# Optimization experiments

Hardware: AMD Instinct MI355X
Metric: run time of the kernel (lower is better)

## Reference

```python
import jax, jax.numpy as jnp
import numpy as np

B, S, D = 8, 2048, 128

def setup_inputs() -> dict:
    key = jax.random.key(0)
    kq, kk, kv, km = jax.random.split(key, 4)
    q = jax.random.normal(kq, (B, S, D), dtype=jnp.float32)
    k = jax.random.normal(kk, (B, S, D), dtype=jnp.float32)
    v = jax.random.normal(kv, (B, S, D), dtype=jnp.float32)
    mask = jax.random.randint(km, (B, S), 0, 2).astype(bool)  # True = masked out
    return {"q": q, "k": k, "v": v, "mask": mask}

def reference(q, k, v, mask):
    scaler = np.sqrt(D).astype(np.float32)
    # score[b, i, j] = <q_i, k_j> / sqrt(d_k)
    score = jnp.einsum('bik,bjk->bij', q, k) / scaler
    score = score - jnp.max(score, axis=-1, keepdims=True)
    e = jnp.exp(score)
    # mask is (B, S_kv): broadcast across query positions, zero out masked keys
    e = jnp.where(mask[:, None, :], 0.0, e)
    a = e / jnp.sum(e, axis=-1, keepdims=True)
    c = jnp.einsum('bij,bjd->bid', a, v)
    return c
```

## Files before the change

kernel.cpp:

```cpp
#include <hip/hip_runtime.h>
#include <hip/hip_fp16.h>
#include <math.h>

typedef __attribute__((ext_vector_type(8))) short short8;
typedef __attribute__((ext_vector_type(16))) float floatx16;
typedef __attribute__((ext_vector_type(2))) __bf16 bf16x2;
typedef __attribute__((ext_vector_type(2))) unsigned int uint2v;

namespace {
constexpr int Bn = 8;
constexpr int Sn = 2048;
constexpr int Dn = 128;
constexpr int BQ = 128;
constexpr int BK = 64;
constexpr int QTILES = Sn / BQ;
constexpr int NKB = Sn / BK;
constexpr int ROWS = Bn * Sn;
constexpr int NSPLIT = 4;
constexpr float SC2 = 0.12753102063642597f;
constexpr float DEFER_THR = 8.0f;
constexpr int TILE_USH = BK * Dn;
}

#if __has_builtin(__builtin_amdgcn_exp2f)
#define EXP2(x) __builtin_amdgcn_exp2f(x)
#else
#define EXP2(x) exp2f(x)
#endif

__device__ __forceinline__ unsigned short f2bf(float x) {
  union { float f; unsigned u; } a; a.f = x;
  unsigned r = a.u + 0x7fffu + ((a.u >> 16) & 1u);
  return (unsigned short)(r >> 16);
}

__device__ __forceinline__ unsigned pack2bf(float x, float y) {
  union { bf16x2 b; unsigned u; } c;
  c.b[0] = (__bf16)x; c.b[1] = (__bf16)y;
  return c.u;
}

__device__ __forceinline__ uint2v pl32swap(unsigned a, unsigned b, int h) {
#if __has_builtin(__builtin_amdgcn_permlane32_swap)
  (void)h;
  return __builtin_amdgcn_permlane32_swap(a, b, false, false);
#else
  unsigned ax = __shfl_xor((int)a, 32);
  unsigned bx = __shfl_xor((int)b, 32);
  uint2v r;
  r[0] = h ? bx : a;
  r[1] = h ? b : ax;
  return r;
#endif
}

__device__ __forceinline__ void gl_lds16(const void* g, void* l, int lane) {
#if __has_builtin(__builtin_amdgcn_global_load_lds)
  (void)lane;
  __builtin_amdgcn_global_load_lds((const __attribute__((address_space(1))) unsigned int*)g,
                                   (__attribute__((address_space(3))) unsigned int*)l, 16, 0, 0);
#else
  *(float4*)((char*)l + lane * 16) = *(const float4*)g;
#endif
}

__global__ __launch_bounds__(256)
void mask_scan(const unsigned char* __restrict__ mraw,
               unsigned short* __restrict__ idxg, int* __restrict__ cntg,
               float* __restrict__ mb2g) {
  __shared__ int sc[256];
  const int b = blockIdx.x;
  const int t = threadIdx.x;

  unsigned wv = ((const unsigned int*)mraw)[t];
  int any1  = __syncthreads_or((wv & 0x0000ff00u) ? 1 : 0);
  int any23 = __syncthreads_or((wv & 0xffff0000u) ? 1 : 0);
  const int mlayout = any1 ? 1 : (any23 ? 2 : 0);

  const int s0 = t * 8;
  const int gbase = b * Sn + s0;
  bool ms[8];
  if (mlayout == 1) {
    #pragma unroll
    for (int i = 0; i < 8; ++i) ms[i] = mraw[gbase + i] != 0;
  } else if (mlayout == 2) {
    const float* mf = (const float*)mraw;
    #pragma unroll
    for (int i = 0; i < 8; ++i) ms[i] = mf[gbase + i] != 0.0f;
  } else {
    const int* mi = (const int*)mraw;
    #pragma unroll
    for (int i = 0; i < 8; ++i) ms[i] = mi[gbase + i] != 0;
  }

  int c = 0;
  #pragma unroll
  for (int i = 0; i < 8; ++i) c += ms[i] ? 0 : 1;
  sc[t] = c;
  __syncthreads();
  for (int off = 1; off < 256; off <<= 1) {
    int v = (t >= off) ? sc[t - off] : 0;
    __syncthreads();
    sc[t] += v;
    __syncthreads();
  }
  const int incl = sc[t];
  const int total = sc[255];
  int pos = incl - c;
  #pragma unroll
  for (int i = 0; i < 8; ++i)
    if (!ms[i]) idxg[b * Sn + (pos++)] = (unsigned short)(s0 + i);
  if (t == 0) cntg[b] = total;
  #pragma unroll
  for (int i = 0; i < 8; ++i)
    mb2g[b * Sn + s0 + i] = (s0 + i < total) ? 0.0f : -1e30f;
}

__global__ __launch_bounds__(256)
void prep(const float* __restrict__ kg, const float* __restrict__ vg,
          const unsigned short* __restrict__ idxg, const int* __restrict__ cntg,
          unsigned short* __restrict__ Kpg, unsigned short* __restrict__ Vpg) {
  __shared__ __align__(16) float Vf[16 * 136];
  const int p = blockIdx.x;
  const int b = p >> 7, qq = p & 127;
  const int kb = qq >> 2, k16 = qq & 3;
  const int t = threadIdx.x;

  const int cnt = cntg[b];
  const int padded = (cnt + 63) & ~63;
  const int slot0 = kb * 64 + k16 * 16;
  if (slot0 >= padded) return;

  const int j  = t >> 4;
  const int o8 = t & 15;
  const int sl = slot0 + j;
  const bool real = sl < cnt;

  float4 a, bq, va, vb;
  if (real) {
    const int srow = idxg[b * Sn + sl];
    const size_t base = ((size_t)(b * Sn + srow)) * 32 + o8 * 2;
    a  = ((const float4*)kg)[base]; bq = ((const float4*)kg)[base + 1];
    va = ((const float4*)vg)[base]; vb = ((const float4*)vg)[base + 1];
  } else {
    a = bq = va = vb = make_float4(0.f, 0.f, 0.f, 0.f);
  }

  {
    union { unsigned u[4]; short8 s8; } pk;
    pk.u[0] = pack2bf(a.x, a.y);   pk.u[1] = pack2bf(a.z, a.w);
    pk.u[2] = pack2bf(bq.x, bq.y); pk.u[3] = pack2bf(bq.z, bq.w);
    const int jl = k16 * 16 + j;
    *(short8*)(Kpg + (size_t)(b * NKB + kb) * TILE_USH + jl * 128 + ((o8 ^ (jl & 7)) * 8)) = pk.s8;
  }
  {
    *(float4*)&Vf[j * 136 + o8 * 8]     = va;
    *(float4*)&Vf[j * 136 + o8 * 8 + 4] = vb;
  }
  __syncthreads();
  {
    const int d = t >> 1, h = t & 1;
    union { unsigned u[4]; short8 s8; } pv;
    #pragma unroll
    for (int i = 0; i < 4; ++i)
      pv.u[i] = pack2bf(Vf[(h * 8 + 2 * i) * 136 + d], Vf[(h * 8 + 2 * i + 1) * 136 + d]);
    const int og = k16 * 2 + h;
    *(short8*)(Vpg + (size_t)(b * NKB + kb) * TILE_USH + d * 64 + ((og ^ (d & 7)) * 8)) = pv.s8;
  }
}


__device__ __forceinline__ void stage_tile(const char* gsrc, char* ldst,
                                           int stagebase, int L) {
  #pragma unroll
  for (int i = 0; i < 4; ++i) {
    const int off = stagebase + i * 1024;
    gl_lds16(gsrc + off + L * 16, ldst + off, L);
  }
}

__device__ __forceinline__ void qk_tile(const unsigned short* __restrict__ Kc,
                                        int q, int h, int sw,
                                        const short8 (&qh)[8], const short8 (&ql)[8],
                                        floatx16 (&s)[2]) {
  #pragma unroll
  for (int kg = 0; kg < 2; ++kg)
    #pragma unroll
    for (int r = 0; r < 16; ++r) s[kg][r] = 0.0f;
  #pragma unroll
  for (int kstep = 0; kstep < 8; ++kstep) {
    const int ko = ((kstep * 2 + h) ^ sw) * 8;
    #pragma unroll
    for (int kg = 0; kg < 2; ++kg) {
      short8 kf = *(const short8*)&Kc[(kg * 32 + q) * 128 + ko];
      s[kg] = __builtin_amdgcn_mfma_f32_32x32x16_bf16(kf, qh[kstep], s[kg], 0, 0, 0);
      s[kg] = __builtin_amdgcn_mfma_f32_32x32x16_bf16(kf, ql[kstep], s[kg], 0, 0, 0);
    }
  }
}

__device__ __forceinline__ void tile_body(
    int kbc, int kbN,
    const unsigned short* __restrict__ Kread, unsigned short* Kdst,
    const unsigned short* __restrict__ Vread, unsigned short* Vdst,
    const char* ktile, const char* vtile, int stagebase, int L,
    const float* __restrict__ mbrow,
    int q, int h, int sw,
    const short8 (&qh)[8], const short8 (&ql)[8],
    floatx16 (&sCur)[2], floatx16 (&sNxt)[2],
    floatx16 (&O32)[4], float& m_i, float& l_i, float& mtrue) {
  __syncthreads();

  if (kbc + 2 < kbN)
    stage_tile(ktile + (size_t)(kbc + 2) * (TILE_USH * 2), (char*)Kdst, stagebase, L);
  const bool hasNext = (kbc + 1 < kbN);
  if (hasNext)
    stage_tile(vtile + (size_t)(kbc + 1) * (TILE_USH * 2), (char*)Vdst, stagebase, L);

  if (hasNext)
    qk_tile(Kread, q, h, sw, qh, ql, sNxt);

  const float4* mb4 = (const float4*)(mbrow + kbc * BK);
  float4 mbv[2][4];
  #pragma unroll
  for (int kg = 0; kg < 2; ++kg)
    #pragma unroll
    for (int ro = 0; ro < 4; ++ro) mbv[kg][ro] = mb4[kg * 8 + ro * 2 + h];

  #pragma unroll
  for (int kg = 0; kg < 2; ++kg)
    #pragma unroll
    for (int ro = 0; ro < 4; ++ro) {
      float4 f = mbv[kg][ro];
      sCur[kg][4 * ro + 0] = fmaf(sCur[kg][4 * ro + 0], SC2, f.x);
      sCur[kg][4 * ro + 1] = fmaf(sCur[kg][4 * ro + 1], SC2, f.y);
      sCur[kg][4 * ro + 2] = fmaf(sCur[kg][4 * ro + 2], SC2, f.z);
      sCur[kg][4 * ro + 3] = fmaf(sCur[kg][4 * ro + 3], SC2, f.w);
    }
  float mxp[4] = {-INFINITY, -INFINITY, -INFINITY, -INFINITY};
  #pragma unroll
  for (int kg = 0; kg < 2; ++kg)
    #pragma unroll
    for (int r = 0; r < 16; ++r) mxp[r & 3] = fmaxf(mxp[r & 3], sCur[kg][r]);
  float mx = fmaxf(fmaxf(mxp[0], mxp[1]), fmaxf(mxp[2], mxp[3]));
  mx = fmaxf(mx, __shfl_xor(mx, 32));
  mtrue = fmaxf(mtrue, mx);

  float mnew;
  if (__all(mx <= m_i + DEFER_THR)) {
    mnew = m_i;
  } else {
    mnew = fmaxf(m_i, mx);
    const float alpha = EXP2(m_i - mnew);
    l_i *= alpha;
    #pragma unroll
    for (int dg = 0; dg < 4; ++dg)
      #pragma unroll
      for (int r = 0; r < 16; ++r) O32[dg][r] *= alpha;
  }

  float rsp[4] = {0.f, 0.f, 0.f, 0.f};
  #pragma unroll
  for (int kg = 0; kg < 2; ++kg)
    #pragma unroll
    for (int r = 0; r < 16; ++r) {
      float e = EXP2(sCur[kg][r] - mnew);
      sCur[kg][r] = e;
      rsp[r & 3] += e;
    }
  float rs = (rsp[0] + rsp[1]) + (rsp[2] + rsp[3]);
  rs += __shfl_xor(rs, 32);
  l_i += rs;
  m_i = mnew;

  unsigned xw[2][4][2];
  #pragma unroll
  for (int kg = 0; kg < 2; ++kg)
    #pragma unroll
    for (int m = 0; m < 4; ++m) {
      xw[kg][m][0] = pack2bf(sCur[kg][4 * m + 0], sCur[kg][4 * m + 1]);
      xw[kg][m][1] = pack2bf(sCur[kg][4 * m + 2], sCur[kg][4 * m + 3]);
    }
  unsigned pfw[4][4];
  #pragma unroll
  for (int kg = 0; kg < 2; ++kg)
    #pragma unroll
    for (int j = 0; j < 2; ++j)
      #pragma unroll
      for (int c2 = 0; c2 < 2; ++c2) {
        uint2v r = pl32swap(xw[kg][2 * j][c2], xw[kg][2 * j + 1][c2], h);
        pfw[kg * 2 + j][c2]     = r[0];
        pfw[kg * 2 + j][2 + c2] = r[1];
      }

  __builtin_amdgcn_s_setprio(1);
  #pragma unroll
  for (int k2 = 0; k2 < 4; ++k2) {
    const int ko = ((k2 * 2 + h) ^ sw) * 8;
    union { unsigned u[4]; short8 s8; } pw;
    pw.u[0] = pfw[k2][0]; pw.u[1] = pfw[k2][1];
    pw.u[2] = pfw[k2][2]; pw.u[3] = pfw[k2][3];
    #pragma unroll
    for (int dg = 0; dg < 4; ++dg) {
      short8 vf = *(const short8*)&Vread[(dg * 32 + q) * 64 + ko];
      O32[dg] = __builtin_amdgcn_mfma_f32_32x32x16_bf16(vf, pw.s8, O32[dg], 0, 0, 0);
    }
  }
  __builtin_amdgcn_s_setprio(0);
}

template<int SPLIT, bool DIRECT>
__global__ __launch_bounds__(256, 2)
void attn_fwd(const float* __restrict__ qg,
              const unsigned short* __restrict__ Kpg,
              const unsigned short* __restrict__ Vpg,
              const float* __restrict__ mb2g,
              const int* __restrict__ cntg,
              float* __restrict__ outg, __half* __restrict__ Op,
              float* __restrict__ Mp, float* __restrict__ Lp) {
  __shared__ __align__(16) unsigned short Khi[2][TILE_USH];
  __shared__ __align__(16) unsigned short Vt[2][TILE_USH];

  const int tid = threadIdx.x;
  const int bid = blockIdx.x;
  const int b   = bid & 7;
  const int q0  = ((bid >> 3) & (QTILES - 1)) * BQ;
  const int s   = bid >> 7;
  const int w   = tid >> 6;
  const int L   = tid & 63;
  const int q   = L & 31;
  const int h   = L >> 5;
  const int sw  = q & 7;

  const int cnt = cntg[b];
  const int nt  = (cnt + 63) >> 6;
  const int kb0 = (s * nt) / SPLIT;
  const int kbN = ((s + 1) * nt) / SPLIT;
  const int T   = kbN - kb0;

  const int row = b * Sn + q0 + w * 32 + q;

  if (T <= 0) {
    if constexpr (DIRECT) {
      float* orow = outg + (size_t)row * Dn;
      float4 z = make_float4(0.f, 0.f, 0.f, 0.f);
      #pragma unroll
      for (int dg = 0; dg < 4; ++dg)
        #pragma unroll
        for (int ro = 0; ro < 4; ++ro) *(float4*)&orow[dg * 32 + 8 * ro + 4 * h] = z;
    } else {
      __half* orow = Op + ((size_t)s * ROWS + row) * Dn;
      uint2 z; z.x = 0u; z.y = 0u;
      #pragma unroll
      for (int dg = 0; dg < 4; ++dg)
        #pragma unroll
        for (int ro = 0; ro < 4; ++ro) *(uint2*)&orow[dg * 32 + 8 * ro + 4 * h] = z;
      if (h == 0) { Mp[s * ROWS + row] = -INFINITY; Lp[s * ROWS + row] = 0.0f; }
    }
    return;
  }

  const char* ktile = (const char*)(Kpg + (size_t)b * NKB * TILE_USH);
  const char* vtile = (const char*)(Vpg + (size_t)b * NKB * TILE_USH);
  const float* mbrow = mb2g + b * Sn;
  const int stagebase = w * 4096;

  short8 qh[8], ql[8];
  {
    const float* qrow = qg + (size_t)row * Dn;
    #pragma unroll
    for (int kstep = 0; kstep < 8; ++kstep) {
      float4 f0 = *(const float4*)(qrow + kstep * 16 + h * 8);
      float4 f1 = *(const float4*)(qrow + kstep * 16 + h * 8 + 4);
      float xs[8] = {f0.x, f0.y, f0.z, f0.w, f1.x, f1.y, f1.z, f1.w};
      #pragma unroll
      for (int j = 0; j < 8; ++j) {
        unsigned short hi = f2bf(xs[j]);
        union { unsigned u; float f; } hv; hv.u = ((unsigned)hi) << 16;
        qh[kstep][j] = (short)hi;
        ql[kstep][j] = (short)f2bf(xs[j] - hv.f);
      }
    }
  }

  float m_i = -INFINITY, l_i = 0.0f;
  float mtrue = -INFINITY;
  floatx16 O32[4];
  #pragma unroll
  for (int dg = 0; dg < 4; ++dg)
    #pragma unroll
    for (int r = 0; r < 16; ++r) O32[dg][r] = 0.0f;

  stage_tile(ktile + (size_t)kb0 * (TILE_USH * 2), (char*)Khi[0], stagebase, L);
  stage_tile(vtile + (size_t)kb0 * (TILE_USH * 2), (char*)Vt[0], stagebase, L);
  __syncthreads();
  if (kb0 + 1 < kbN)
    stage_tile(ktile + (size_t)(kb0 + 1) * (TILE_USH * 2), (char*)Khi[1], stagebase, L);

  floatx16 sA[2], sB[2];
  qk_tile(Khi[0], q, h, sw, qh, ql, sA);

  int kb = kb0;
  for (; kb + 2 <= kbN; kb += 2) {
    tile_body(kb, kbN, Khi[1], Khi[0], Vt[0], Vt[1], ktile, vtile, stagebase, L,
              mbrow, q, h, sw, qh, ql, sA, sB, O32, m_i, l_i, mtrue);
    tile_body(kb + 1, kbN, Khi[0], Khi[1], Vt[1], Vt[0], ktile, vtile, stagebase, L,
              mbrow, q, h, sw, qh, ql, sB, sA, O32, m_i, l_i, mtrue);
  }
  if (kb < kbN)
    tile_body(kb, kbN, Khi[1], Khi[0], Vt[0], Vt[1], ktile, vtile, stagebase, L,
              mbrow, q, h, sw, qh, ql, sA, sB, O32, m_i, l_i, mtrue);

  if constexpr (DIRECT) {
    const float inv = 1.0f / l_i;
    float* orow = outg + (size_t)row * Dn;
    #pragma unroll
    for (int dg = 0; dg < 4; ++dg)
      #pragma unroll
      for (int ro = 0; ro < 4; ++ro) {
        float4 f = make_float4(O32[dg][4 * ro] * inv,     O32[dg][4 * ro + 1] * inv,
                               O32[dg][4 * ro + 2] * inv, O32[dg][4 * ro + 3] * inv);
        *(float4*)&orow[dg * 32 + 8 * ro + 4 * h] = f;
      }
  } else {
    const float fin = EXP2(m_i - mtrue);
    __half* orow = Op + ((size_t)s * ROWS + row) * Dn;
    #pragma unroll
    for (int dg = 0; dg < 4; ++dg)
      #pragma unroll
      for (int ro = 0; ro < 4; ++ro) {
        union { __half2 h2[2]; uint2 u; } pk;
        pk.h2[0] = __floats2half2_rn(O32[dg][4 * ro] * fin,     O32[dg][4 * ro + 1] * fin);
        pk.h2[1] = __floats2half2_rn(O32[dg][4 * ro + 2] * fin, O32[dg][4 * ro + 3] * fin);
        *(uint2*)&orow[dg * 32 + 8 * ro + 4 * h] = pk.u;
      }
    if (h == 0) {
      Mp[s * ROWS + row] = mtrue;
      Lp[s * ROWS + row] = l_i * fin;
    }
  }
}

__global__ __launch_bounds__(256)
void attn_combine(const __half* __restrict__ Op, const float* __restrict__ Mp,
                  const float* __restrict__ Lp, float4* __restrict__ out4) {
  const int gid = blockIdx.x * 256 + threadIdx.x;
  const int row = gid >> 5;
  const int c4  = gid & 31;
  float ms[NSPLIT];
  float m = -INFINITY;
  #pragma unroll
  for (int s = 0; s < NSPLIT; ++s) { ms[s] = Mp[s * ROWS + row]; m = fmaxf(m, ms[s]); }
  float l = 0.0f;
  float4 acc = make_float4(0.f, 0.f, 0.f, 0.f);
  #pragma unroll
  for (int s = 0; s < NSPLIT; ++s) {
    float wgt = EXP2(ms[s] - m);
    l = fmaf(Lp[s * ROWS + row], wgt, l);
    union { uint2 u; __half2 h2[2]; } pk;
    pk.u = ((const uint2*)Op)[(size_t)(s * ROWS + row) * 32 + c4];
    float2 f0 = __half22float2(pk.h2[0]);
    float2 f1 = __half22float2(pk.h2[1]);
    acc.x = fmaf(f0.x, wgt, acc.x);
    acc.y = fmaf(f0.y, wgt, acc.y);
    acc.z = fmaf(f1.x, wgt, acc.z);
    acc.w = fmaf(f1.y, wgt, acc.w);
  }
  float inv = 1.0f / l;
  out4[(size_t)row * 32 + c4] = make_float4(acc.x * inv, acc.y * inv, acc.z * inv, acc.w * inv);
}

extern "C" void kernel_launch(void* const* d_in, const int* in_sizes, int n_in,
                              void* d_out, int out_size, void* d_ws, size_t ws_size,
                              hipStream_t stream) {
  const float* q = (const float*)d_in[0];
  const float* k = (const float*)d_in[1];
  const float* v = (const float*)d_in[2];
  const unsigned char* m = (const unsigned char*)d_in[3];
  float* out = (float*)d_out;
  (void)in_sizes; (void)n_in; (void)out_size;

  constexpr size_t OPB = (size_t)NSPLIT * ROWS * Dn * sizeof(__half);
  constexpr size_t MLB = (size_t)NSPLIT * ROWS * sizeof(float);
  constexpr size_t KPB = (size_t)Bn * NKB * TILE_USH * 2;
  constexpr size_t MBB = (size_t)ROWS * sizeof(float);
  constexpr size_t CNTB = 64;
  constexpr size_t IDXB = (size_t)Bn * Sn * sizeof(unsigned short);

  char* ws = (char*)d_ws;
  if (ws_size >= OPB + 2 * MLB + 2 * KPB + MBB + CNTB + IDXB) {
    __half* Op = (__half*)ws;
    float* Mp = (float*)(ws + OPB);
    float* Lp = (float*)(ws + OPB + MLB);
    unsigned short* Kp = (unsigned short*)(ws + OPB + 2 * MLB);
    unsigned short* Vp = (unsigned short*)(ws + OPB + 2 * MLB + KPB);
    float* mb2 = (float*)(ws + OPB + 2 * MLB + 2 * KPB);
    int* cnt = (int*)(ws + OPB + 2 * MLB + 2 * KPB + MBB);
    unsigned short* idx = (unsigned short*)(ws + OPB + 2 * MLB + 2 * KPB + MBB + CNTB);
    mask_scan<<<dim3(Bn), dim3(256), 0, stream>>>(m, idx, cnt, mb2);
    prep<<<dim3(Bn * NKB * 4), dim3(256), 0, stream>>>(k, v, idx, cnt, Kp, Vp);
    attn_fwd<NSPLIT, false><<<dim3(Bn * QTILES * NSPLIT), dim3(256), 0, stream>>>(
        q, Kp, Vp, mb2, cnt, out, Op, Mp, Lp);
    attn_combine<<<dim3(ROWS * 32 / 256), dim3(256), 0, stream>>>(
        Op, Mp, Lp, (float4*)out);
  } else if (ws_size >= 2 * KPB + MBB + CNTB + IDXB) {
    unsigned short* Kp = (unsigned short*)ws;
    unsigned short* Vp = (unsigned short*)(ws + KPB);
    float* mb2 = (float*)(ws + 2 * KPB);
    int* cnt = (int*)(ws + 2 * KPB + MBB);
    unsigned short* idx = (unsigned short*)(ws + 2 * KPB + MBB + CNTB);
    mask_scan<<<dim3(Bn), dim3(256), 0, stream>>>(m, idx, cnt, mb2);
    prep<<<dim3(Bn * NKB * 4), dim3(256), 0, stream>>>(k, v, idx, cnt, Kp, Vp);
    attn_fwd<1, true><<<dim3(Bn * QTILES), dim3(256), 0, stream>>>(
        q, Kp, Vp, mb2, cnt, out, nullptr, nullptr, nullptr);
  }
}
```

Baseline: 110.1 us.

## Fuse mask scan into prep kernel and compute key padding mask inline

Removes the separate mask_scan launch: every prep block now redoes the per-batch prefix scan over the mask and keeps only the 16 compacted indices it needs in shared memory. The attention kernel drops the per-tile mask-bias loads and derives the padding bias from the valid-key count, using a plain scale on full tiles. This saves one kernel launch, a serial dependency and the global idx/mb2 traffic, at the cost of repeating the scan in 1024 blocks.

New measurement: 116.3 us. 5.7% more time.

```diff
diff --git a/kernel.cpp b/kernel.cpp
--- a/kernel.cpp
+++ b/kernel.cpp
@@ -65,11 +65,16 @@
 }
 
 __global__ __launch_bounds__(256)
-void mask_scan(const unsigned char* __restrict__ mraw,
-               unsigned short* __restrict__ idxg, int* __restrict__ cntg,
-               float* __restrict__ mb2g) {
+void prep(const float* __restrict__ kg, const float* __restrict__ vg,
+          const unsigned char* __restrict__ mraw,
+          unsigned short* __restrict__ Kpg, unsigned short* __restrict__ Vpg,
+          int* __restrict__ cntg) {
   __shared__ int sc[256];
-  const int b = blockIdx.x;
+  __shared__ unsigned short idxl[16];
+  __shared__ __align__(16) float Vf[16 * 136];
+  const int p = blockIdx.x;
+  const int b = p >> 7, qq = p & 127;
+  const int kb = qq >> 2, k16 = qq & 3;
   const int t = threadIdx.x;
 
   unsigned wv = ((const unsigned int*)mraw)[t];
@@ -106,39 +111,29 @@
   }
   const int incl = sc[t];
   const int total = sc[255];
+  const int slot0 = kb * 64 + k16 * 16;
+
   int pos = incl - c;
   #pragma unroll
   for (int i = 0; i < 8; ++i)
-    if (!ms[i]) idxg[b * Sn + (pos++)] = (unsigned short)(s0 + i);
-  if (t == 0) cntg[b] = total;
-  #pragma unroll
-  for (int i = 0; i < 8; ++i)
-    mb2g[b * Sn + s0 + i] = (s0 + i < total) ? 0.0f : -1e30f;
-}
-
-__global__ __launch_bounds__(256)
-void prep(const float* __restrict__ kg, const float* __restrict__ vg,
-          const unsigned short* __restrict__ idxg, const int* __restrict__ cntg,
-          unsigned short* __restrict__ Kpg, unsigned short* __restrict__ Vpg) {
-  __shared__ __align__(16) float Vf[16 * 136];
-  const int p = blockIdx.x;
-  const int b = p >> 7, qq = p & 127;
-  const int kb = qq >> 2, k16 = qq & 3;
-  const int t = threadIdx.x;
-
-  const int cnt = cntg[b];
-  const int padded = (cnt + 63) & ~63;
-  const int slot0 = kb * 64 + k16 * 16;
+    if (!ms[i]) {
+      if (pos >= slot0 && pos < slot0 + 16) idxl[pos - slot0] = (unsigned short)(s0 + i);
+      ++pos;
+    }
+  if (qq == 0 && t == 0) cntg[b] = total;
+
+  const int padded = (total + 63) & ~63;
+  __syncthreads();
   if (slot0 >= padded) return;
 
   const int j  = t >> 4;
   const int o8 = t & 15;
   const int sl = slot0 + j;
-  const bool real = sl < cnt;
+  const bool real = sl < total;
 
   float4 a, bq, va, vb;
   if (real) {
-    const int srow = idxg[b * Sn + sl];
+    const int srow = idxl[j];
     const size_t base = ((size_t)(b * Sn + srow)) * 32 + o8 * 2;
     a  = ((const float4*)kg)[base]; bq = ((const float4*)kg)[base + 1];
     va = ((const float4*)vg)[base]; vb = ((const float4*)vg)[base + 1];
@@ -204,7 +199,7 @@
     const unsigned short* __restrict__ Kread, unsigned short* Kdst,
     const unsigned short* __restrict__ Vread, unsigned short* Vdst,
     const char* ktile, const char* vtile, int stagebase, int L,
-    const float* __restrict__ mbrow,
+    int cnt,
     int q, int h, int sw,
     const short8 (&qh)[8], const short8 (&ql)[8],
     floatx16 (&sCur)[2], floatx16 (&sNxt)[2],
@@ -220,23 +215,20 @@
   if (hasNext)
     qk_tile(Kread, q, h, sw, qh, ql, sNxt);
 
-  const float4* mb4 = (const float4*)(mbrow + kbc * BK);
-  float4 mbv[2][4];
-  #pragma unroll
-  for (int kg = 0; kg < 2; ++kg)
-    #pragma unroll
-    for (int ro = 0; ro < 4; ++ro) mbv[kg][ro] = mb4[kg * 8 + ro * 2 + h];
-
-  #pragma unroll
-  for (int kg = 0; kg < 2; ++kg)
-    #pragma unroll
-    for (int ro = 0; ro < 4; ++ro) {
-      float4 f = mbv[kg][ro];
-      sCur[kg][4 * ro + 0] = fmaf(sCur[kg][4 * ro + 0], SC2, f.x);
-      sCur[kg][4 * ro + 1] = fmaf(sCur[kg][4 * ro + 1], SC2, f.y);
-      sCur[kg][4 * ro + 2] = fmaf(sCur[kg][4 * ro + 2], SC2, f.z);
-      sCur[kg][4 * ro + 3] = fmaf(sCur[kg][4 * ro + 3], SC2, f.w);
-    }
+  if ((kbc + 1) * BK <= cnt) {
+    #pragma unroll
+    for (int kg = 0; kg < 2; ++kg)
+      #pragma unroll
+      for (int r = 0; r < 16; ++r) sCur[kg][r] *= SC2;
+  } else {
+    #pragma unroll
+    for (int kg = 0; kg < 2; ++kg)
+      #pragma unroll
+      for (int r = 0; r < 16; ++r) {
+        const int key = kbc * BK + kg * 32 + ((r & 3) + 8 * (r >> 2)) + 4 * h;
+        sCur[kg][r] = fmaf(sCur[kg][r], SC2, (key < cnt) ? 0.0f : -1e30f);
+      }
+  }
   float mxp[4] = {-INFINITY, -INFINITY, -INFINITY, -INFINITY};
   #pragma unroll
   for (int kg = 0; kg < 2; ++kg)
@@ -314,7 +306,6 @@
 void attn_fwd(const float* __restrict__ qg,
               const unsigned short* __restrict__ Kpg,
               const unsigned short* __restrict__ Vpg,
-              const float* __restrict__ mb2g,
               const int* __restrict__ cntg,
               float* __restrict__ outg, __half* __restrict__ Op,
               float* __restrict__ Mp, float* __restrict__ Lp) {
@@ -362,7 +353,6 @@
 
   const char* ktile = (const char*)(Kpg + (size_t)b * NKB * TILE_USH);
   const char* vtile = (const char*)(Vpg + (size_t)b * NKB * TILE_USH);
-  const float* mbrow = mb2g + b * Sn;
   const int stagebase = w * 4096;
 
   short8 qh[8], ql[8];
@@ -403,13 +393,13 @@
   int kb = kb0;
   for (; kb + 2 <= kbN; kb += 2) {
     tile_body(kb, kbN, Khi[1], Khi[0], Vt[0], Vt[1], ktile, vtile, stagebase, L,
-              mbrow, q, h, sw, qh, ql, sA, sB, O32, m_i, l_i, mtrue);
+              cnt, q, h, sw, qh, ql, sA, sB, O32, m_i, l_i, mtrue);
     tile_body(kb + 1, kbN, Khi[0], Khi[1], Vt[1], Vt[0], ktile, vtile, stagebase, L,
-              mbrow, q, h, sw, qh, ql, sB, sA, O32, m_i, l_i, mtrue);
+              cnt, q, h, sw, qh, ql, sB, sA, O32, m_i, l_i, mtrue);
   }
   if (kb < kbN)
     tile_body(kb, kbN, Khi[1], Khi[0], Vt[0], Vt[1], ktile, vtile, stagebase, L,
-              mbrow, q, h, sw, qh, ql, sA, sB, O32, m_i, l_i, mtrue);
+              cnt, q, h, sw, qh, ql, sA, sB, O32, m_i, l_i, mtrue);
 
   if constexpr (DIRECT) {
     const float inv = 1.0f / l_i;
@@ -483,35 +473,27 @@
   constexpr size_t OPB = (size_t)NSPLIT * ROWS * Dn * sizeof(__half);
   constexpr size_t MLB = (size_t)NSPLIT * ROWS * sizeof(float);
   constexpr size_t KPB = (size_t)Bn * NKB * TILE_USH * 2;
-  constexpr size_t MBB = (size_t)ROWS * sizeof(float);
   constexpr size_t CNTB = 64;
-  constexpr size_t IDXB = (size_t)Bn * Sn * sizeof(unsigned short);
 
   char* ws = (char*)d_ws;
-  if (ws_size >= OPB + 2 * MLB + 2 * KPB + MBB + CNTB + IDXB) {
+  if (ws_size >= OPB + 2 * MLB + 2 * KPB + CNTB) {
     __half* Op = (__half*)ws;
     float* Mp = (float*)(ws + OPB);
     float* Lp = (float*)(ws + OPB + MLB);
     unsigned short* Kp = (unsigned short*)(ws + OPB + 2 * MLB);
     unsigned short* Vp = (unsigned short*)(ws + OPB + 2 * MLB + KPB);
-    float* mb2 = (float*)(ws + OPB + 2 * MLB + 2 * KPB);
-    int* cnt = (int*)(ws + OPB + 2 * MLB + 2 * KPB + MBB);
-    unsigned short* idx = (unsigned short*)(ws + OPB + 2 * MLB + 2 * KPB + MBB + CNTB);
-    mask_scan<<<dim3(Bn), dim3(256), 0, stream>>>(m, idx, cnt, mb2);
-    prep<<<dim3(Bn * NKB * 4), dim3(256), 0, stream>>>(k, v, idx, cnt, Kp, Vp);
+    int* cnt = (int*)(ws + OPB + 2 * MLB + 2 * KPB);
+    prep<<<dim3(Bn * NKB * 4), dim3(256), 0, stream>>>(k, v, m, Kp, Vp, cnt);
     attn_fwd<NSPLIT, false><<<dim3(Bn * QTILES * NSPLIT), dim3(256), 0, stream>>>(
-        q, Kp, Vp, mb2, cnt, out, Op, Mp, Lp);
+        q, Kp, Vp, cnt, out, Op, Mp, Lp);
     attn_combine<<<dim3(ROWS * 32 / 256), dim3(256), 0, stream>>>(
         Op, Mp, Lp, (float4*)out);
-  } else if (ws_size >= 2 * KPB + MBB + CNTB + IDXB) {
+  } else if (ws_size >= 2 * KPB + CNTB) {
     unsigned short* Kp = (unsigned short*)ws;
     unsigned short* Vp = (unsigned short*)(ws + KPB);
-    float* mb2 = (float*)(ws + 2 * KPB);
-    int* cnt = (int*)(ws + 2 * KPB + MBB);
-    unsigned short* idx = (unsigned short*)(ws + 2 * KPB + MBB + CNTB);
-    mask_scan<<<dim3(Bn), dim3(256), 0, stream>>>(m, idx, cnt, mb2);
-    prep<<<dim3(Bn * NKB * 4), dim3(256), 0, stream>>>(k, v, idx, cnt, Kp, Vp);
+    int* cnt = (int*)(ws + 2 * KPB);
+    prep<<<dim3(Bn * NKB * 4), dim3(256), 0, stream>>>(k, v, m, Kp, Vp, cnt);
     attn_fwd<1, true><<<dim3(Bn * QTILES), dim3(256), 0, stream>>>(
-        q, Kp, Vp, mb2, cnt, out, nullptr, nullptr, nullptr);
-  }
-}
+        q, Kp, Vp, cnt, out, nullptr, nullptr, nullptr);
+  }
+}
```
